# Optimization experiments

Hardware: AMD Instinct MI355X
Metric: run time of the kernel (lower is better)

The kernel has to match this reference:

```python
import jax, jax.numpy as jnp
import numpy as np

N, R, H0, H1, E, NB = 50000, 16, 128, 64, 800000, 8


def setup_inputs() -> dict:
    key = jax.random.key(0)
    k = jax.random.split(key, 6)
    nodes = jax.random.normal(k[0], (N, H0), dtype=jnp.float32)
    comps = jax.random.normal(k[1], (R, NB), dtype=jnp.float32) * 0.1
    bases = jax.random.normal(k[2], (NB, H0, H1), dtype=jnp.float32) * 0.05
    bias = jnp.zeros((H1,), dtype=jnp.float32)
    src = jax.random.randint(k[3], (E,), 0, N)
    rel = jax.random.randint(k[4], (E,), 0, R)
    dst = jax.random.randint(k[5], (E,), 0, N)
    return {"nodes": nodes, "comps": comps, "bases": bases, "bias": bias,
            "src": src, "rel": rel, "dst": dst}


def reference(nodes, comps, bases, bias, src, rel, dst):
    n, h0 = nodes.shape
    r = comps.shape[0]
    # Edge normalization: util.sum_sparse on the VERTICAL stacking -> row index
    # is rel*n + src, so each edge value is 1 / (#edges with same (rel, subject)).
    row = rel * n + src  # (E,)
    counts = jax.ops.segment_sum(jnp.ones(src.shape, jnp.float32), row, num_segments=r * n)
    vals = 1.0 / counts[row]  # (E,)
    # Basis decomposition: weights[r] = sum_b comps[r,b] * bases[b]
    weights = jnp.einsum('rb,bio->rio', comps, bases)  # (r, h0, h1)
    # Per-relation transformed node features (equivalent to expand + 'rni,rio->rno')
    nw = jnp.einsum('ni,rio->rno', nodes, weights)  # (r, n, h1)
    # Horizontal sparse mm: out[s] += val * nw[rel, dst]
    msgs = nw[rel, dst] * vals[:, None]  # (E, h1) gather
    out = jax.ops.segment_sum(msgs, src, num_segments=n)  # (n, h1) scatter-add
    return out + bias
```

## Files before the change

### kernel.cpp

```cpp
#include <hip/hip_runtime.h>
#include <hip/hip_bf16.h>

#define NN 50000
#define RR 16
#define H0 128
#define H1 64
#define EE 800000
#define NBASE 8
#define NTILES (NN / 16)
#define NGRPS ((NTILES + 3) / 4)
#define GEMM_BLOCKS NGRPS
#define COUNT_BLOCKS ((EE + 255) / 256)
#define NM (NN * RR)
#define NB1 782

typedef __attribute__((ext_vector_type(8))) short short8;
typedef __attribute__((ext_vector_type(4))) float f32x4;

__device__ inline short f2bs(float x) {
    __hip_bfloat16 b = __float2bfloat16(x);
    return *reinterpret_cast<short*>(&b);
}

__global__ void k_prep(const float* __restrict__ comps, const float* __restrict__ bases,
                       __hip_bfloat16* __restrict__ wtT, int* __restrict__ cnt) {
    if (blockIdx.x < 512) {
        int idx = blockIdx.x * 256 + threadIdx.x;
        int r = idx / (H1 * H0);
        int rem = idx % (H1 * H0);
        int o = rem / H0;
        int i = rem % H0;
        float acc = 0.0f;
#pragma unroll
        for (int b = 0; b < NBASE; ++b)
            acc += comps[r * NBASE + b] * bases[(b * H0 + i) * H1 + o];
        wtT[idx] = __float2bfloat16(acc);
    } else {
        int g = (blockIdx.x - 512) * 256 + threadIdx.x;
        if (g * 4 < NM) *(int4*)&cnt[g * 4] = (int4){0, 0, 0, 0};
    }
}

__global__ __launch_bounds__(256, 1)
void k_fused(const float* __restrict__ nodes,
             const __hip_bfloat16* __restrict__ wtT,
             __hip_bfloat16* __restrict__ nw,
             const int* __restrict__ src, const int* __restrict__ rel,
             int* __restrict__ cnt, int* __restrict__ rank) {
    if (blockIdx.x < GEMM_BLOCKS) {
        int wid  = threadIdx.x >> 6;
        int lane = threadIdx.x & 63;
        int gw   = blockIdx.x * 4 + wid;
        int ngrp = gw >> 2;
        int rg   = gw & 3;
        int n16  = lane & 15;
        int kg   = lane >> 4;

        int ntl = NTILES - ngrp * 4;
        if (ntl > 4) ntl = 4;

        short8 afrag[4][4];
#pragma unroll
        for (int t = 0; t < 4; ++t) {
            if (t < ntl) {
                const float* ap = &nodes[(size_t)((ngrp * 4 + t) * 16 + n16) * H0 + kg * 8];
#pragma unroll
                for (int ks = 0; ks < 4; ++ks) {
                    float4 lo = *(const float4*)(ap + ks * 32);
                    float4 hi = *(const float4*)(ap + ks * 32 + 4);
                    short8 a;
                    a[0] = f2bs(lo.x); a[1] = f2bs(lo.y); a[2] = f2bs(lo.z); a[3] = f2bs(lo.w);
                    a[4] = f2bs(hi.x); a[5] = f2bs(hi.y); a[6] = f2bs(hi.z); a[7] = f2bs(hi.w);
                    afrag[t][ks] = a;
                }
            }
        }

        int chb = (n16 >> 2) * 16 + (n16 & 3);

        for (int r0 = 0; r0 < 4; ++r0) {
            int r = rg * 4 + r0;
            const __hip_bfloat16* wrr = &wtT[((size_t)r * H1 + chb) * H0 + kg * 8];
            f32x4 acc[4][4];
#pragma unroll
            for (int ot = 0; ot < 4; ++ot)
#pragma unroll
                for (int t = 0; t < 4; ++t) acc[ot][t] = (f32x4){0, 0, 0, 0};

#pragma unroll
            for (int ot = 0; ot < 4; ++ot) {
#pragma unroll
                for (int ks = 0; ks < 4; ++ks) {
                    short8 w = *(const short8*)(wrr + (size_t)(ot * 4) * H0 + ks * 32);
                    acc[ot][0] = __builtin_amdgcn_mfma_f32_16x16x32_bf16(w, afrag[0][ks], acc[ot][0], 0, 0, 0);
                    acc[ot][1] = __builtin_amdgcn_mfma_f32_16x16x32_bf16(w, afrag[1][ks], acc[ot][1], 0, 0, 0);
                    acc[ot][2] = __builtin_amdgcn_mfma_f32_16x16x32_bf16(w, afrag[2][ks], acc[ot][2], 0, 0, 0);
                    acc[ot][3] = __builtin_amdgcn_mfma_f32_16x16x32_bf16(w, afrag[3][ks], acc[ot][3], 0, 0, 0);
                }
            }

#pragma unroll
            for (int t = 0; t < 4; ++t) {
                if (t >= ntl) break;
                unsigned pk[8];
#pragma unroll
                for (int j = 0; j < 8; ++j) {
                    f32x4 a = acc[j >> 1][t];
                    float lo = a[(j & 1) * 2], hi = a[(j & 1) * 2 + 1];
                    pk[j] = (unsigned)(unsigned short)f2bs(lo) |
                            ((unsigned)(unsigned short)f2bs(hi) << 16);
                }
                uint4 q0; q0.x = pk[0]; q0.y = pk[1]; q0.z = pk[2]; q0.w = pk[3];
                uint4 q1; q1.x = pk[4]; q1.y = pk[5]; q1.z = pk[6]; q1.w = pk[7];
                char* rowp = (char*)nw +
                             ((size_t)r * NN + (size_t)ngrp * 64 + t * 16 + n16) * 128;
                *(uint4*)(rowp + kg * 16)      = q0;
                *(uint4*)(rowp + 64 + kg * 16) = q1;
            }
        }
    } else {
        int e = (blockIdx.x - GEMM_BLOCKS) * 256 + threadIdx.x;
        if (e < EE) {
            int bin = src[e] * RR + rel[e];
            rank[e] = atomicAdd(&cnt[bin], 1);
        }
    }
}

__global__ void k_scan1(const int* __restrict__ cnt, int* __restrict__ base2,
                        int* __restrict__ bsums) {
    __shared__ int tmp[256];
    int tid = threadIdx.x;
    int g = blockIdx.x * 256 + tid;
    int4 v = {0, 0, 0, 0};
    if (g * 4 < NM) v = *(const int4*)&cnt[g * 4];
    int s = v.x + v.y + v.z + v.w;
    tmp[tid] = s;
    __syncthreads();
    for (int off = 1; off < 256; off <<= 1) {
        int t = (tid >= off) ? tmp[tid - off] : 0;
        __syncthreads();
        tmp[tid] += t;
        __syncthreads();
    }
    int excl = tmp[tid] - s;
    if (tid == 255) bsums[blockIdx.x] = tmp[255];
    if (g * 4 < NM) {
        int4 o;
        o.x = excl;
        o.y = excl + v.x;
        o.z = excl + v.x + v.y;
        o.w = excl + v.x + v.y + v.z;
        *(int4*)&base2[g * 4] = o;
    }
}

__global__ void k_scan2(const int* __restrict__ bsums, int* __restrict__ bsofs) {
    __shared__ int tmp[256];
    int t = threadIdx.x;
    int i0 = t * 4;
    int v0 = (i0 < NB1) ? bsums[i0] : 0;
    int v1 = (i0 + 1 < NB1) ? bsums[i0 + 1] : 0;
    int v2 = (i0 + 2 < NB1) ? bsums[i0 + 2] : 0;
    int v3 = (i0 + 3 < NB1) ? bsums[i0 + 3] : 0;
    int tot = v0 + v1 + v2 + v3;
    tmp[t] = tot;
    __syncthreads();
    for (int off = 1; off < 256; off <<= 1) {
        int x = (t >= off) ? tmp[t - off] : 0;
        __syncthreads();
        tmp[t] += x;
        __syncthreads();
    }
    int excl = tmp[t] - tot;
    if (i0 < NB1)     bsofs[i0]     = excl;
    if (i0 + 1 < NB1) bsofs[i0 + 1] = excl + v0;
    if (i0 + 2 < NB1) bsofs[i0 + 2] = excl + v0 + v1;
    if (i0 + 3 < NB1) bsofs[i0 + 3] = excl + v0 + v1 + v2;
}

__global__ void k_place(const int* __restrict__ src, const int* __restrict__ rel,
                        const int* __restrict__ dst, const int* __restrict__ base2,
                        const int* __restrict__ bsofs, const int* __restrict__ rank,
                        unsigned* __restrict__ recs) {
    int e = blockIdx.x * blockDim.x + threadIdx.x;
    if (e < EE) {
        int bin = src[e] * RR + rel[e];
        int pos = base2[bin] + bsofs[bin >> 10] + rank[e];
        recs[pos] = ((unsigned)rel[e] << 16) | (unsigned)dst[e];
    }
}

__global__ void k_accum(const int* __restrict__ cnt, const int* __restrict__ base2,
                        const int* __restrict__ bsofs, const unsigned* __restrict__ recs,
                        const __hip_bfloat16* __restrict__ nw, const float* __restrict__ bias,
                        float* __restrict__ out) {
    __shared__ float inv[4][16];
    int w = threadIdx.x >> 6;
    int s = blockIdx.x * 4 + w;
    int lane = threadIdx.x & 63;
    if (s >= NN) return;
    if (lane < 16) inv[w][lane] = 1.0f / (float)cnt[s * RR + lane];
    int pl = ((lane >> 3) & 1) * 32 + (lane >> 4) * 8 + (lane & 7);
    int i0 = s * RR;
    int b0 = base2[i0] + bsofs[i0 >> 10];
    int b1 = (s == NN - 1) ? EE : base2[i0 + RR] + bsofs[(i0 + RR) >> 10];
    int n = b1 - b0;
    float a0 = bias[lane], a1 = 0.0f, a2 = 0.0f, a3 = 0.0f;
    int i = 0;
    for (; i + 4 <= n; i += 4) {
        unsigned rec0 = recs[b0 + i], rec1 = recs[b0 + i + 1];
        unsigned rec2 = recs[b0 + i + 2], rec3 = recs[b0 + i + 3];
        int r0 = rec0 >> 16, d0 = rec0 & 0xFFFF;
        int r1 = rec1 >> 16, d1 = rec1 & 0xFFFF;
        int r2 = rec2 >> 16, d2 = rec2 & 0xFFFF;
        int r3 = rec3 >> 16, d3 = rec3 & 0xFFFF;
        float m0 = __bfloat162float(nw[((size_t)r0 * NN + d0) * H1 + pl]);
        float m1 = __bfloat162float(nw[((size_t)r1 * NN + d1) * H1 + pl]);
        float m2 = __bfloat162float(nw[((size_t)r2 * NN + d2) * H1 + pl]);
        float m3 = __bfloat162float(nw[((size_t)r3 * NN + d3) * H1 + pl]);
        a0 += inv[w][r0] * m0;
        a1 += inv[w][r1] * m1;
        a2 += inv[w][r2] * m2;
        a3 += inv[w][r3] * m3;
    }
    for (; i < n; ++i) {
        unsigned rec = recs[b0 + i];
        int r = rec >> 16, d = rec & 0xFFFF;
        a0 += inv[w][r] * __bfloat162float(nw[((size_t)r * NN + d) * H1 + pl]);
    }
    out[(size_t)s * H1 + lane] = (a0 + a1) + (a2 + a3);
}

__global__ void k_init_out(float* __restrict__ out, const float* __restrict__ bias) {
    int i = blockIdx.x * blockDim.x + threadIdx.x;
    if (i < NN * H1) out[i] = bias[i & (H1 - 1)];
}

__global__ void k_count_only(const int* __restrict__ src, const int* __restrict__ rel,
                             float* __restrict__ counts) {
    int e = blockIdx.x * blockDim.x + threadIdx.x;
    if (e < EE) atomicAdd(&counts[rel[e] * NN + src[e]], 1.0f);
}

__global__ void k_weights_fb(const float* __restrict__ comps, const float* __restrict__ bases,
                             __hip_bfloat16* __restrict__ wtT) {
    int idx = blockIdx.x * blockDim.x + threadIdx.x;
    if (idx >= RR * H1 * H0) return;
    int r = idx / (H1 * H0);
    int rem = idx % (H1 * H0);
    int o = rem / H0;
    int i = rem % H0;
    float acc = 0.0f;
#pragma unroll
    for (int b = 0; b < NBASE; ++b)
        acc += comps[r * NBASE + b] * bases[(b * H0 + i) * H1 + o];
    wtT[idx] = __float2bfloat16(acc);
}

__global__ void k_fused_edge(const int* __restrict__ src, const int* __restrict__ rel,
                             const int* __restrict__ dst, const float* __restrict__ nodes,
                             const float* __restrict__ counts,
                             const __hip_bfloat16* __restrict__ wtT, float* __restrict__ out) {
    int e = blockIdx.x * (blockDim.x >> 6) + (threadIdx.x >> 6);
    int lane = threadIdx.x & 63;
    if (e >= EE) return;
    int s = src[e], r = rel[e], d = dst[e];
    float val = 1.0f / counts[r * NN + s];
    const __hip_bfloat16* w = &wtT[(size_t)(r * H1 + lane) * H0];
    const float* nd = &nodes[(size_t)d * H0];
    float acc = 0.0f;
#pragma unroll 8
    for (int i = 0; i < H0; ++i) acc += nd[i] * __bfloat162float(w[i]);
    atomicAdd(&out[s * H1 + lane], acc * val);
}

extern "C" void kernel_launch(void* const* d_in, const int* in_sizes, int n_in,
                              void* d_out, int out_size, void* d_ws, size_t ws_size,
                              hipStream_t stream) {
    const float* nodes = (const float*)d_in[0];
    const float* comps = (const float*)d_in[1];
    const float* bases = (const float*)d_in[2];
    const float* bias  = (const float*)d_in[3];
    const int*   src   = (const int*)d_in[4];
    const int*   rel   = (const int*)d_in[5];
    const int*   dst   = (const int*)d_in[6];
    float* out = (float*)d_out;

    char* ws = (char*)d_ws;
    int*   cnt           = (int*)ws;
    int*   base2         = (int*)(ws + 3200256);
    int*   bsums         = (int*)(ws + 6400512);
    int*   bsofs         = (int*)(ws + 6403968);
    __hip_bfloat16* wtT  = (__hip_bfloat16*)(ws + 6407424);
    int*   rank          = (int*)(ws + 6669824);
    unsigned* recs       = (unsigned*)(ws + 9870080);
    __hip_bfloat16* nw   = (__hip_bfloat16*)(ws + 13070080);
    const size_t need_full = 13070080ull + (size_t)RR * NN * H1 * 2ull;

    if (ws_size >= need_full) {
        k_prep<<<512 + 782, 256, 0, stream>>>(comps, bases, wtT, cnt);
        k_fused<<<GEMM_BLOCKS + COUNT_BLOCKS, 256, 0, stream>>>(nodes, wtT, nw, src, rel, cnt, rank);
        k_scan1<<<NB1, 256, 0, stream>>>(cnt, base2, bsums);
        k_scan2<<<1, 256, 0, stream>>>(bsums, bsofs);
        k_place<<<(EE + 255) / 256, 256, 0, stream>>>(src, rel, dst, base2, bsofs, rank, recs);
        k_accum<<<(NN + 3) / 4, 256, 0, stream>>>(cnt, base2, bsofs, recs, nw, bias, out);
    } else {
        float* countsF = (float*)ws;
        __hip_bfloat16* wtT2 = (__hip_bfloat16*)(ws + 3200256);
        (void)hipMemsetAsync(countsF, 0, (size_t)NM * 4, stream);
        k_count_only<<<(EE + 255) / 256, 256, 0, stream>>>(src, rel, countsF);
        k_weights_fb<<<(RR * H1 * H0 + 255) / 256, 256, 0, stream>>>(comps, bases, wtT2);
        k_init_out<<<(NN * H1 + 255) / 256, 256, 0, stream>>>(out, bias);
        k_fused_edge<<<EE / 4, 256, 0, stream>>>(src, rel, dst, nodes, countsF, wtT2, out);
    }
}
```

Baseline: 134.9 us.

## Stage bf16 node tile in shared memory once per block for all relation groups

Previously each of the four waves in a GEMM block loaded and converted the same 64-node fp32 tile from global memory, since the waves only differed by relation group. Now the whole block cooperatively loads the tile once, converts it to bf16, and writes it to an XOR-swizzled LDS buffer. Each wave then reads its A fragments from LDS. This cuts redundant global reads and conversions by about four times, at the cost of 16KB of LDS, a barrier, and an LDS round trip.

```diff
diff --git a/kernel.cpp b/kernel.cpp
--- a/kernel.cpp
+++ b/kernel.cpp
@@ -15,6 +15,7 @@
 #define NB1 782
 
 typedef __attribute__((ext_vector_type(8))) short short8;
+typedef __attribute__((ext_vector_type(4))) short short4v;
 typedef __attribute__((ext_vector_type(4))) float f32x4;
 
 __device__ inline short f2bs(float x) {
@@ -47,32 +48,43 @@
              __hip_bfloat16* __restrict__ nw,
              const int* __restrict__ src, const int* __restrict__ rel,
              int* __restrict__ cnt, int* __restrict__ rank) {
+    __shared__ __hip_bfloat16 asmem[64 * 128];
     if (blockIdx.x < GEMM_BLOCKS) {
-        int wid  = threadIdx.x >> 6;
-        int lane = threadIdx.x & 63;
-        int gw   = blockIdx.x * 4 + wid;
-        int ngrp = gw >> 2;
-        int rg   = gw & 3;
+        int tid  = threadIdx.x;
+        int ngrp = blockIdx.x;
+        int ntl = NTILES - ngrp * 4;
+        if (ntl > 4) ntl = 4;
+
+#pragma unroll
+        for (int i = 0; i < 8; ++i) {
+            int f = i * 256 + tid;
+            int row = f >> 5;
+            int chunk = f & 31;
+            int node = ngrp * 64 + row;
+            if (node > NN - 1) node = NN - 1;
+            float4 v = *(const float4*)&nodes[(size_t)node * H0 + chunk * 4];
+            short4v o;
+            o[0] = f2bs(v.x); o[1] = f2bs(v.y); o[2] = f2bs(v.z); o[3] = f2bs(v.w);
+            int blk = chunk >> 1, half = chunk & 1;
+            *(short4v*)((char*)asmem + row * 256 + ((blk ^ (row & 7)) << 4) + half * 8) = o;
+        }
+        __syncthreads();
+
+        int wid  = tid >> 6;
+        int lane = tid & 63;
+        int rg   = wid;
         int n16  = lane & 15;
         int kg   = lane >> 4;
 
-        int ntl = NTILES - ngrp * 4;
-        if (ntl > 4) ntl = 4;
-
         short8 afrag[4][4];
 #pragma unroll
         for (int t = 0; t < 4; ++t) {
             if (t < ntl) {
-                const float* ap = &nodes[(size_t)((ngrp * 4 + t) * 16 + n16) * H0 + kg * 8];
-#pragma unroll
-                for (int ks = 0; ks < 4; ++ks) {
-                    float4 lo = *(const float4*)(ap + ks * 32);
-                    float4 hi = *(const float4*)(ap + ks * 32 + 4);
-                    short8 a;
-                    a[0] = f2bs(lo.x); a[1] = f2bs(lo.y); a[2] = f2bs(lo.z); a[3] = f2bs(lo.w);
-                    a[4] = f2bs(hi.x); a[5] = f2bs(hi.y); a[6] = f2bs(hi.z); a[7] = f2bs(hi.w);
-                    afrag[t][ks] = a;
-                }
+                int r = t * 16 + n16;
+#pragma unroll
+                for (int ks = 0; ks < 4; ++ks)
+                    afrag[t][ks] = *(const short8*)((char*)asmem + r * 256 +
+                                                    (((ks * 4 + kg) ^ (n16 & 7)) << 4));
             }
         }
 
```

After: 128.6 us. 4.6% less time.
